# Optimization experiments

Measured on AMD Instinct MI355X. Metric: run time of the kernel, lower is better.

## Reference

```python
import jax, jax.numpy as jnp
import numpy as np

N_NODES = 50000
N_EDGES = 800000
N_GRAPHS = 512
IN_FEATS = 256
HIDDEN = 128
OUT_FEATS = 128


def _lin(key, fan_in, fan_out):
    return jax.random.normal(key, (fan_in, fan_out), jnp.float32) * (1.0 / np.sqrt(fan_in))


def setup_inputs() -> dict:
    key = jax.random.key(0)
    ks = jax.random.split(key, 16)
    x = jax.random.normal(ks[0], (N_NODES, IN_FEATS), jnp.float32)
    edge_index = jax.random.randint(ks[1], (2, N_EDGES), 0, N_NODES, jnp.int32)
    batch = jnp.sort(jax.random.randint(ks[2], (N_NODES,), 0, N_GRAPHS, jnp.int32))
    return {
        "x": x,
        "edge_index": edge_index,
        "batch": batch,
        "num_graphs": N_GRAPHS,
        # TD branch GCN params
        "td_W1": _lin(ks[3], IN_FEATS, HIDDEN), "td_b1": jnp.zeros((HIDDEN,), jnp.float32),
        "td_W2": _lin(ks[4], HIDDEN, OUT_FEATS), "td_b2": jnp.zeros((OUT_FEATS,), jnp.float32),
        # BU branch GCN params
        "bu_W1": _lin(ks[5], IN_FEATS, HIDDEN), "bu_b1": jnp.zeros((HIDDEN,), jnp.float32),
        "bu_W2": _lin(ks[6], HIDDEN, OUT_FEATS), "bu_b2": jnp.zeros((OUT_FEATS,), jnp.float32),
        # proj_head: Linear(256,256) -> ReLU -> Linear(256,128)
        "pw1": _lin(ks[7], OUT_FEATS * 2, 256), "pb1": jnp.zeros((256,), jnp.float32),
        "pw2": _lin(ks[8], 256, 128), "pb2": jnp.zeros((128,), jnp.float32),
    }


def gcn_conv(h_in, W, b, src, dst, n_nodes):
    """PyG GCNConv: self-loops + symmetric normalization D^-1/2 (A+I) D^-1/2 X W + b."""
    h = h_in @ W  # [N, out]
    ones = jnp.ones(src.shape[0], h.dtype)
    deg = jax.ops.segment_sum(ones, dst, num_segments=n_nodes) + 1.0  # +1 for self-loop
    dinv = jax.lax.rsqrt(deg)  # deg >= 1 always
    norm = dinv[src] * dinv[dst]  # [E]
    agg = jax.ops.segment_sum(h[src] * norm[:, None], dst, num_segments=n_nodes)
    agg = agg + h * (dinv * dinv)[:, None]  # self-loop edge contribution
    return agg + b


def reference(x, edge_index, batch, num_graphs,
              td_W1, td_b1, td_W2, td_b2,
              bu_W1, bu_b1, bu_W2, bu_b2,
              pw1, pb1, pw2, pb2):
    n = x.shape[0]
    src, dst = edge_index[0], edge_index[1]

    def branch(W1, b1, W2, b2, s, d):
        h = jax.nn.relu(gcn_conv(x, W1, b1, s, d, n))
        # dropout is identity in eval mode
        h = gcn_conv(h, W2, b2, s, d, n)
        return jax.ops.segment_sum(h, batch, num_segments=num_graphs)  # global_add_pool

    td = branch(td_W1, td_b1, td_W2, td_b2, src, dst)
    bu = branch(bu_W1, bu_b1, bu_W2, bu_b2, dst, src)  # flipped edge_index
    h = jnp.concatenate([bu, td], axis=1)  # [G, 2*out_feats]
    h = jax.nn.relu(h @ pw1 + pb1) @ pw2 + pb2
    return h
```

## Files before the change

### kernel.cpp

```cpp
#include <hip/hip_runtime.h>

#define N_NODES 50000
#define N_PAD   50048
#define N_EDGES 800000
#define N_GRAPHS 512
#define F_IN 256
#define F_H 128
#define F_CAT 256

#define BSHIFT 9
#define NB 98
#define CAP 10240
#define EPB 3125

typedef __attribute__((ext_vector_type(8))) short short8;
typedef __attribute__((ext_vector_type(4))) float f32x4;
typedef unsigned int uint;
typedef unsigned short ushort;

static __device__ __forceinline__ ushort f2bf(float f) {
    uint u = __float_as_uint(f);
    u += 0x7FFF + ((u >> 16) & 1);
    return (ushort)(u >> 16);
}
static __device__ __forceinline__ float bflo(uint v) { return __uint_as_float(v << 16); }
static __device__ __forceinline__ float bfhi(uint v) { return __uint_as_float(v & 0xFFFF0000u); }

#define GLL(g, l) __builtin_amdgcn_global_load_lds( \
    (const __attribute__((address_space(1))) unsigned int*)(g), \
    (__attribute__((address_space(3))) unsigned int*)(l), 16, 0, 0)

__global__ void init_gcur_kernel(int* gcur) {
    int t = threadIdx.x;
    if (t < 2 * NB) gcur[t] = (t % NB) * CAP;
}

__global__ __launch_bounds__(256) void csr_scatter_kernel(
        const int* __restrict__ ei, int* __restrict__ gcur,
        uint* __restrict__ ebuf_td, uint* __restrict__ ebuf_bu) {
    __shared__ int lcnt[256];
    __shared__ int lbase[256];
    int tid = threadIdx.x;
    lcnt[tid] = 0;
    __syncthreads();
    int e0 = blockIdx.x * EPB;
    for (int k = tid; k < EPB; k += 256) {
        int i = e0 + k;
        int s = ei[i], d = ei[N_EDGES + i];
        atomicAdd(&lcnt[d >> BSHIFT], 1);
        atomicAdd(&lcnt[128 + (s >> BSHIFT)], 1);
    }
    __syncthreads();
    if (tid < 2 * NB) {
        int dir = tid / NB, b = tid % NB;
        int c = lcnt[dir * 128 + b];
        lbase[dir * 128 + b] = c ? atomicAdd(&gcur[dir * NB + b], c) : 0;
    }
    __syncthreads();
    lcnt[tid] = 0;
    __syncthreads();
    for (int k = tid; k < EPB; k += 256) {
        int i = e0 + k;
        int s = ei[i], d = ei[N_EDGES + i];
        int bd = d >> BSHIFT, bs = s >> BSHIFT;
        int p = atomicAdd(&lcnt[bd], 1) + lbase[bd];
        ebuf_td[p] = (uint)s | ((uint)(d & 511) << 16);
        int q = atomicAdd(&lcnt[128 + bs], 1) + lbase[128 + bs];
        ebuf_bu[q] = (uint)d | ((uint)(s & 511) << 16);
    }
}

__global__ __launch_bounds__(256) void csr_build_kernel(
        const uint* __restrict__ ebuf_td, const uint* __restrict__ ebuf_bu,
        const int* __restrict__ gcur,
        int* off_td, int* off_bu, ushort* deg_td, ushort* deg_bu,
        float* dinv_td, float* dinv_bu, ushort* csr_td, ushort* csr_bu) {
    int b = blockIdx.x, dir = blockIdx.y;
    const uint* ebuf = dir ? ebuf_bu : ebuf_td;
    int* off     = dir ? off_bu : off_td;
    ushort* deg  = dir ? deg_bu : deg_td;
    float* dinv  = dir ? dinv_bu : dinv_td;
    ushort* csr  = dir ? csr_bu : csr_td;
    __shared__ int cntL[512], offL[512], sm[256];
    int tid = threadIdx.x;
    cntL[tid] = 0; cntL[tid + 256] = 0;
    __syncthreads();
    int rbeg = b * CAP;
    int rend = gcur[dir * NB + b];
    for (int k = rbeg + tid; k < rend; k += 256)
        atomicAdd(&cntL[ebuf[k] >> 16], 1);
    __syncthreads();
    int a0 = cntL[tid * 2], a1 = cntL[tid * 2 + 1];
    int ps = a0 + a1;
    sm[tid] = ps;
    __syncthreads();
    for (int o = 1; o < 256; o <<= 1) {
        int u = (tid >= o) ? sm[tid - o] : 0;
        __syncthreads();
        sm[tid] += u;
        __syncthreads();
    }
    int excl = sm[tid] - ps;
    offL[tid * 2] = excl;
    offL[tid * 2 + 1] = excl + a0;
    __syncthreads();
    int nbase = b << BSHIFT;
#pragma unroll
    for (int j = 0; j < 2; j++) {
        int nloc = tid + j * 256;
        int n = nbase + nloc;
        if (n < N_NODES) {
            off[n] = rbeg + offL[nloc];
            int c = cntL[nloc];
            deg[n] = (ushort)c;
            dinv[n] = rsqrtf((float)c + 1.0f);
        }
    }
    cntL[tid] = offL[tid];
    cntL[tid + 256] = offL[tid + 256];
    __syncthreads();
    for (int k = rbeg + tid; k < rend; k += 256) {
        uint e = ebuf[k];
        int slot = atomicAdd(&cntL[e >> 16], 1);
        csr[rbeg + slot] = (ushort)(e & 0xFFFF);
    }
}

__global__ void cvt_x_kernel(const float* __restrict__ x, ushort* __restrict__ xb) {
    size_t i = (size_t)blockIdx.x * blockDim.x + threadIdx.x;
    ushort4 u = {0, 0, 0, 0};
    if (i < (size_t)N_NODES * (F_IN / 4)) {
        float4 f = ((const float4*)x)[i];
        u.x = f2bf(f.x); u.y = f2bf(f.y); u.z = f2bf(f.z); u.w = f2bf(f.w);
    }
    ((ushort4*)xb)[i] = u;
}

__global__ void prep_w_kernel(const float* __restrict__ td_W1, const float* __restrict__ bu_W1,
                              const float* __restrict__ td_W2, const float* __restrict__ bu_W2,
                              ushort* __restrict__ Bt1, ushort* __restrict__ Bt2) {
    int n = blockIdx.x;
    int k = threadIdx.x;
    float w1 = (n < F_H) ? td_W1[(size_t)k * F_H + n] : bu_W1[(size_t)k * F_H + (n - F_H)];
    Bt1[(size_t)n * 256 + k] = f2bf(w1);
    if (k < 128) {
        float w2 = (n < F_H) ? td_W2[(size_t)k * F_H + n]
                             : bu_W2[(size_t)k * F_H + (n - F_H)];
        Bt2[(size_t)n * 128 + k] = f2bf(w2);
    }
}

__global__ __launch_bounds__(256) void gemm_mfma(
        const ushort* __restrict__ A, const ushort* __restrict__ Bt,
        ushort* __restrict__ C,
        const float* __restrict__ dinv_td, const float* __restrict__ dinv_bu,
        int kLen, int ldb, int aSplit) {
    __shared__ __align__(16) ushort As[128 * 32];
    __shared__ __align__(16) ushort Bs[128 * 32];
    int tid = threadIdx.x;
    int wave = tid >> 6, lane = tid & 63, quad = lane >> 4, l16 = lane & 15;
    size_t bm = (size_t)blockIdx.x * 128;
    size_t bn = (size_t)blockIdx.y * 128;
    const float* dsel = blockIdx.y ? dinv_bu : dinv_td;
    int aOff = aSplit ? (int)bn : 0;

    f32x4 acc[2][8];
    const f32x4 z4 = {0.f, 0.f, 0.f, 0.f};
#pragma unroll
    for (int i = 0; i < 2; i++)
#pragma unroll
        for (int j = 0; j < 8; j++) acc[i][j] = z4;

    int cb0 = wave * 64;
    int cb1 = 256 + wave * 64;
    int c0 = cb0 + lane, c1 = cb1 + lane;
    int r0 = c0 >> 2, s0 = (c0 & 3) * 8;
    int r1 = c1 >> 2, s1 = (c1 & 3) * 8;
    const ushort* a0p = A + (bm + r0) * 256 + aOff + s0;
    const ushort* a1p = A + (bm + r1) * 256 + aOff + s1;
    const ushort* b0p = Bt + (bn + r0) * ldb + s0;
    const ushort* b1p = Bt + (bn + r1) * ldb + s1;
    ushort* lA0 = As + cb0 * 8;
    ushort* lA1 = As + cb1 * 8;
    ushort* lB0 = Bs + cb0 * 8;
    ushort* lB1 = Bs + cb1 * 8;

    int nkb = kLen >> 5;
    for (int kb = 0; kb < nkb; kb++) {
        int k0 = kb * 32;
        __syncthreads();
        GLL(a0p + k0, lA0);
        GLL(a1p + k0, lA1);
        GLL(b0p + k0, lB0);
        GLL(b1p + k0, lB1);
        __syncthreads();
        short8 af0 = *(const short8*)(As + (wave * 32 + l16) * 32 + quad * 8);
        short8 af1 = *(const short8*)(As + (wave * 32 + 16 + l16) * 32 + quad * 8);
#pragma unroll
        for (int ct = 0; ct < 8; ct++) {
            short8 bfr = *(const short8*)(Bs + (ct * 16 + l16) * 32 + quad * 8);
            acc[0][ct] = __builtin_amdgcn_mfma_f32_16x16x32_bf16(af0, bfr, acc[0][ct], 0, 0, 0);
            acc[1][ct] = __builtin_amdgcn_mfma_f32_16x16x32_bf16(af1, bfr, acc[1][ct], 0, 0, 0);
        }
    }
#pragma unroll
    for (int rt = 0; rt < 2; rt++) {
#pragma unroll
        for (int r = 0; r < 4; r++) {
            size_t row = bm + wave * 32 + rt * 16 + quad * 4 + r;
            float dv = dsel[row];
#pragma unroll
            for (int ct = 0; ct < 8; ct++) {
                C[row * 256 + bn + ct * 16 + l16] = f2bf(acc[rt][ct][r] * dv);
            }
        }
    }
}

static __device__ __forceinline__ void gather_row(const ushort* __restrict__ base,
                                                  const ushort* __restrict__ csr,
                                                  int s, int e, float& a0, float& a1) {
    float p0 = 0, p1 = 0, q0 = 0, q1 = 0, r0 = 0, r1 = 0;
    int k = s;
    for (; k + 4 <= e; k += 4) {
        int i0 = csr[k], i1 = csr[k + 1], i2 = csr[k + 2], i3 = csr[k + 3];
        uint v0 = *(const uint*)(base + (size_t)i0 * F_CAT);
        uint v1 = *(const uint*)(base + (size_t)i1 * F_CAT);
        uint v2 = *(const uint*)(base + (size_t)i2 * F_CAT);
        uint v3 = *(const uint*)(base + (size_t)i3 * F_CAT);
        a0 += bflo(v0); a1 += bfhi(v0);
        p0 += bflo(v1); p1 += bfhi(v1);
        q0 += bflo(v2); q1 += bfhi(v2);
        r0 += bflo(v3); r1 += bfhi(v3);
    }
    for (; k < e; k++) {
        int i0 = csr[k];
        uint v0 = *(const uint*)(base + (size_t)i0 * F_CAT);
        a0 += bflo(v0); a1 += bfhi(v0);
    }
    a0 += (p0 + q0) + r0;
    a1 += (p1 + q1) + r1;
}

__global__ __launch_bounds__(128) void agg1_kernel(
        const ushort* __restrict__ linS, ushort* __restrict__ h1b,
        const ushort* __restrict__ csr_td, const int* __restrict__ off_td,
        const ushort* __restrict__ deg_td, const float* __restrict__ dinv_td,
        const ushort* __restrict__ csr_bu, const int* __restrict__ off_bu,
        const ushort* __restrict__ deg_bu, const float* __restrict__ dinv_bu,
        const float* __restrict__ b_td, const float* __restrict__ b_bu) {
    int n = blockIdx.x;
    int br = threadIdx.x >> 6, lane = threadIdx.x & 63;
    const ushort* csr = br ? csr_bu : csr_td;
    const int* off    = br ? off_bu : off_td;
    const ushort* deg = br ? deg_bu : deg_td;
    const float* dinv = br ? dinv_bu : dinv_td;
    const float* bias = br ? b_bu : b_td;
    size_t cbase = (size_t)br * F_H + lane * 2;
    const ushort* base = linS + cbase;

    uint v = *(const uint*)(base + (size_t)n * F_CAT);
    float a0 = bflo(v), a1 = bfhi(v);
    int s = off[n];
    gather_row(base, csr, s, s + deg[n], a0, a1);
    float dn = dinv[n];
    float o0 = fmaxf(a0 * dn + bias[lane * 2], 0.f);
    float o1 = fmaxf(a1 * dn + bias[lane * 2 + 1], 0.f);
    uint pk = (uint)f2bf(o0) | ((uint)f2bf(o1) << 16);
    *(uint*)(h1b + (size_t)n * F_CAT + cbase) = pk;
}

__global__ __launch_bounds__(128) void agg2_pool_kernel(
        const ushort* __restrict__ linS, float* __restrict__ pooled,
        const int* __restrict__ batch,
        const ushort* __restrict__ csr_td, const int* __restrict__ off_td,
        const ushort* __restrict__ deg_td, const float* __restrict__ dinv_td,
        const ushort* __restrict__ csr_bu, const int* __restrict__ off_bu,
        const ushort* __restrict__ deg_bu, const float* __restrict__ dinv_bu,
        const float* __restrict__ b_td, const float* __restrict__ b_bu) {
    int n0 = blockIdx.x * 8;
    int br = threadIdx.x >> 6, lane = threadIdx.x & 63;
    const ushort* csr = br ? csr_bu : csr_td;
    const int* off    = br ? off_bu : off_td;
    const ushort* deg = br ? deg_bu : deg_td;
    const float* dinv = br ? dinv_bu : dinv_td;
    const float* bias = br ? b_bu : b_td;
    size_t cbase = (size_t)br * F_H + lane * 2;
    const ushort* base = linS + cbase;
    int pcol = (br ? 0 : F_H) + lane * 2;
    float bs0 = bias[lane * 2], bs1 = bias[lane * 2 + 1];

    float acc0 = 0.f, acc1 = 0.f;
    int gcur = batch[n0];
#pragma unroll
    for (int j = 0; j < 8; j++) {
        int n = n0 + j;
        int g = batch[n];
        if (g != gcur) {
            unsafeAtomicAdd(&pooled[(size_t)gcur * F_CAT + pcol], acc0);
            unsafeAtomicAdd(&pooled[(size_t)gcur * F_CAT + pcol + 1], acc1);
            acc0 = acc1 = 0.f;
            gcur = g;
        }
        uint v = *(const uint*)(base + (size_t)n * F_CAT);
        float a0 = bflo(v), a1 = bfhi(v);
        int s = off[n];
        gather_row(base, csr, s, s + deg[n], a0, a1);
        float dn = dinv[n];
        acc0 += a0 * dn + bs0;
        acc1 += a1 * dn + bs1;
    }
    unsafeAtomicAdd(&pooled[(size_t)gcur * F_CAT + pcol], acc0);
    unsafeAtomicAdd(&pooled[(size_t)gcur * F_CAT + pcol + 1], acc1);
}

__global__ __launch_bounds__(256) void mlp_kernel(const float* __restrict__ pooled,
                                                  const float* __restrict__ pw1,
                                                  const float* __restrict__ pb1,
                                                  const float* __restrict__ pw2,
                                                  const float* __restrict__ pb2,
                                                  float* __restrict__ out) {
    int g = blockIdx.x;
    int tid = threadIdx.x;
    __shared__ float row[256];
    __shared__ float hid[256];
    row[tid] = pooled[(size_t)g * 256 + tid];
    __syncthreads();
    float acc = pb1[tid];
    for (int k = 0; k < 256; k++) acc += row[k] * pw1[(size_t)k * 256 + tid];
    hid[tid] = fmaxf(acc, 0.f);
    __syncthreads();
    if (tid < 128) {
        float o = pb2[tid];
        for (int k = 0; k < 256; k++) o += hid[k] * pw2[(size_t)k * 128 + tid];
        out[(size_t)g * 128 + tid] = o;
    }
}

extern "C" void kernel_launch(void* const* d_in, const int* in_sizes, int n_in,
                              void* d_out, int out_size, void* d_ws, size_t ws_size,
                              hipStream_t stream) {
    const float* x     = (const float*)d_in[0];
    const int*   ei    = (const int*)d_in[1];
    const int*   batch = (const int*)d_in[2];
    const float* td_W1 = (const float*)d_in[4];
    const float* td_b1 = (const float*)d_in[5];
    const float* td_W2 = (const float*)d_in[6];
    const float* td_b2 = (const float*)d_in[7];
    const float* bu_W1 = (const float*)d_in[8];
    const float* bu_b1 = (const float*)d_in[9];
    const float* bu_W2 = (const float*)d_in[10];
    const float* bu_b2 = (const float*)d_in[11];
    const float* pw1   = (const float*)d_in[12];
    const float* pb1   = (const float*)d_in[13];
    const float* pw2   = (const float*)d_in[14];
    const float* pb2   = (const float*)d_in[15];
    float* out = (float*)d_out;

    char* p = (char*)d_ws;
    auto alloc = [&](size_t bytes) { void* r = (void*)p; p += (bytes + 255) & ~(size_t)255; return r; };
    int* gcur = (int*)alloc(2 * NB * sizeof(int));
    uint* ebuf_td = (uint*)alloc((size_t)NB * CAP * sizeof(uint));
    uint* ebuf_bu = (uint*)alloc((size_t)NB * CAP * sizeof(uint));
    ushort* csr_td = (ushort*)alloc((size_t)NB * CAP * sizeof(ushort));
    ushort* csr_bu = (ushort*)alloc((size_t)NB * CAP * sizeof(ushort));
    int* off_td = (int*)alloc((size_t)N_NODES * sizeof(int));
    int* off_bu = (int*)alloc((size_t)N_NODES * sizeof(int));
    ushort* deg_td = (ushort*)alloc((size_t)N_NODES * sizeof(ushort));
    ushort* deg_bu = (ushort*)alloc((size_t)N_NODES * sizeof(ushort));
    float* dinv_td = (float*)alloc((size_t)N_PAD * sizeof(float));
    float* dinv_bu = (float*)alloc((size_t)N_PAD * sizeof(float));
    ushort* Bt1 = (ushort*)alloc((size_t)256 * 256 * sizeof(ushort));
    ushort* Bt2 = (ushort*)alloc((size_t)256 * 128 * sizeof(ushort));
    ushort* xb   = (ushort*)alloc((size_t)N_PAD * F_CAT * sizeof(ushort));
    ushort* linb = (ushort*)alloc((size_t)N_PAD * F_CAT * sizeof(ushort));
    ushort* h1b  = (ushort*)alloc((size_t)N_PAD * F_CAT * sizeof(ushort));
    float* pooled = (float*)alloc((size_t)N_GRAPHS * F_CAT * sizeof(float));

    hipMemsetAsync(pooled, 0, (size_t)N_GRAPHS * F_CAT * sizeof(float), stream);

    init_gcur_kernel<<<1, 256, 0, stream>>>(gcur);
    csr_scatter_kernel<<<N_EDGES / EPB, 256, 0, stream>>>(ei, gcur, ebuf_td, ebuf_bu);
    csr_build_kernel<<<dim3(NB, 2), 256, 0, stream>>>(ebuf_td, ebuf_bu, gcur,
        off_td, off_bu, deg_td, deg_bu, dinv_td, dinv_bu, csr_td, csr_bu);

    cvt_x_kernel<<<(N_PAD * F_IN / 4) / 256, 256, 0, stream>>>(x, xb);
    prep_w_kernel<<<256, 256, 0, stream>>>(td_W1, bu_W1, td_W2, bu_W2, Bt1, Bt2);

    dim3 gg(N_PAD / 128, 2);

    gemm_mfma<<<gg, 256, 0, stream>>>(xb, Bt1, linb, dinv_td, dinv_bu, 256, 256, 0);
    agg1_kernel<<<N_NODES, 128, 0, stream>>>(linb, h1b,
        csr_td, off_td, deg_td, dinv_td, csr_bu, off_bu, deg_bu, dinv_bu, td_b1, bu_b1);

    gemm_mfma<<<gg, 256, 0, stream>>>(h1b, Bt2, linb, dinv_td, dinv_bu, 128, 128, 1);
    agg2_pool_kernel<<<N_NODES / 8, 128, 0, stream>>>(linb, pooled, batch,
        csr_td, off_td, deg_td, dinv_td, csr_bu, off_bu, deg_bu, dinv_bu, td_b2, bu_b2);

    mlp_kernel<<<N_GRAPHS, 256, 0, stream>>>(pooled, pw1, pb1, pw2, pb2, out);
}
```

Baseline: 372.1 us.

## Split aggregation columns into 32-wide slices with edge-parallel lanes per wave

The aggregation kernels now give each wave one node (or 8-node group) and one 32-column slice. The 64 lanes are split into 4 edge sub-groups of 16 column lanes, and partial sums are combined with cross-lane shuffles. The aim is more memory-level parallelism per node, since 8 edges are loaded concurrently per step instead of one row per lane serially, and better spread of work across blocks. The cost is 64-byte row segments per gather instead of 256-byte ones, idle lanes on low-degree tails, and reloading CSR indices 8 times per node.

```diff
diff --git a/kernel.cpp b/kernel.cpp
--- a/kernel.cpp
+++ b/kernel.cpp
@@ -217,60 +217,51 @@
     }
 }
 
-static __device__ __forceinline__ void gather_row(const ushort* __restrict__ base,
-                                                  const ushort* __restrict__ csr,
-                                                  int s, int e, float& a0, float& a1) {
-    float p0 = 0, p1 = 0, q0 = 0, q1 = 0, r0 = 0, r1 = 0;
-    int k = s;
-    for (; k + 4 <= e; k += 4) {
-        int i0 = csr[k], i1 = csr[k + 1], i2 = csr[k + 2], i3 = csr[k + 3];
-        uint v0 = *(const uint*)(base + (size_t)i0 * F_CAT);
-        uint v1 = *(const uint*)(base + (size_t)i1 * F_CAT);
-        uint v2 = *(const uint*)(base + (size_t)i2 * F_CAT);
-        uint v3 = *(const uint*)(base + (size_t)i3 * F_CAT);
-        a0 += bflo(v0); a1 += bfhi(v0);
-        p0 += bflo(v1); p1 += bfhi(v1);
-        q0 += bflo(v2); q1 += bfhi(v2);
-        r0 += bflo(v3); r1 += bfhi(v3);
-    }
-    for (; k < e; k++) {
-        int i0 = csr[k];
-        uint v0 = *(const uint*)(base + (size_t)i0 * F_CAT);
-        a0 += bflo(v0); a1 += bfhi(v0);
-    }
-    a0 += (p0 + q0) + r0;
-    a1 += (p1 + q1) + r1;
-}
-
-__global__ __launch_bounds__(128) void agg1_kernel(
+__global__ __launch_bounds__(256) void agg1_kernel(
         const ushort* __restrict__ linS, ushort* __restrict__ h1b,
         const ushort* __restrict__ csr_td, const int* __restrict__ off_td,
         const ushort* __restrict__ deg_td, const float* __restrict__ dinv_td,
         const ushort* __restrict__ csr_bu, const int* __restrict__ off_bu,
         const ushort* __restrict__ deg_bu, const float* __restrict__ dinv_bu,
         const float* __restrict__ b_td, const float* __restrict__ b_bu) {
-    int n = blockIdx.x;
-    int br = threadIdx.x >> 6, lane = threadIdx.x & 63;
-    const ushort* csr = br ? csr_bu : csr_td;
-    const int* off    = br ? off_bu : off_td;
-    const ushort* deg = br ? deg_bu : deg_td;
-    const float* dinv = br ? dinv_bu : dinv_td;
-    const float* bias = br ? b_bu : b_td;
-    size_t cbase = (size_t)br * F_H + lane * 2;
-    const ushort* base = linS + cbase;
-
-    uint v = *(const uint*)(base + (size_t)n * F_CAT);
-    float a0 = bflo(v), a1 = bfhi(v);
-    int s = off[n];
-    gather_row(base, csr, s, s + deg[n], a0, a1);
+    int s = blockIdx.x & 7;
+    int wave = threadIdx.x >> 6, lane = threadIdx.x & 63;
+    int n = (blockIdx.x >> 3) * 4 + wave;
+    int dir = s >> 2;
+    const ushort* csr = dir ? csr_bu : csr_td;
+    const int* off    = dir ? off_bu : off_td;
+    const ushort* deg = dir ? deg_bu : deg_td;
+    const float* dinv = dir ? dinv_bu : dinv_td;
+    const float* bias = dir ? b_bu : b_td;
+    int e_sub = lane >> 4, c_sub = lane & 15;
+    int col = s * 32 + c_sub * 2;
+    const ushort* base = linS + col;
+
+    float a0 = 0.f, a1 = 0.f;
+    int kb = off[n], ke = kb + deg[n];
+    for (int k = kb; k < ke; k += 8) {
+        int k1 = k + e_sub, k2 = k + 4 + e_sub;
+        uint v1 = 0, v2 = 0;
+        if (k1 < ke) v1 = *(const uint*)(base + (size_t)csr[k1] * F_CAT);
+        if (k2 < ke) v2 = *(const uint*)(base + (size_t)csr[k2] * F_CAT);
+        a0 += bflo(v1) + bflo(v2);
+        a1 += bfhi(v1) + bfhi(v2);
+    }
+    a0 += __shfl_xor(a0, 16); a1 += __shfl_xor(a1, 16);
+    a0 += __shfl_xor(a0, 32); a1 += __shfl_xor(a1, 32);
+    uint vs = *(const uint*)(base + (size_t)n * F_CAT);
+    a0 += bflo(vs); a1 += bfhi(vs);
     float dn = dinv[n];
-    float o0 = fmaxf(a0 * dn + bias[lane * 2], 0.f);
-    float o1 = fmaxf(a1 * dn + bias[lane * 2 + 1], 0.f);
-    uint pk = (uint)f2bf(o0) | ((uint)f2bf(o1) << 16);
-    *(uint*)(h1b + (size_t)n * F_CAT + cbase) = pk;
-}
-
-__global__ __launch_bounds__(128) void agg2_pool_kernel(
+    int bcol = col - dir * F_H;
+    float o0 = fmaxf(a0 * dn + bias[bcol], 0.f);
+    float o1 = fmaxf(a1 * dn + bias[bcol + 1], 0.f);
+    if (e_sub == 0) {
+        uint pk = (uint)f2bf(o0) | ((uint)f2bf(o1) << 16);
+        *(uint*)(h1b + (size_t)n * F_CAT + col) = pk;
+    }
+}
+
+__global__ __launch_bounds__(256) void agg2_pool_kernel(
         const ushort* __restrict__ linS, float* __restrict__ pooled,
         const int* __restrict__ batch,
         const ushort* __restrict__ csr_td, const int* __restrict__ off_td,
@@ -278,17 +269,22 @@
         const ushort* __restrict__ csr_bu, const int* __restrict__ off_bu,
         const ushort* __restrict__ deg_bu, const float* __restrict__ dinv_bu,
         const float* __restrict__ b_td, const float* __restrict__ b_bu) {
-    int n0 = blockIdx.x * 8;
-    int br = threadIdx.x >> 6, lane = threadIdx.x & 63;
-    const ushort* csr = br ? csr_bu : csr_td;
-    const int* off    = br ? off_bu : off_td;
-    const ushort* deg = br ? deg_bu : deg_td;
-    const float* dinv = br ? dinv_bu : dinv_td;
-    const float* bias = br ? b_bu : b_td;
-    size_t cbase = (size_t)br * F_H + lane * 2;
-    const ushort* base = linS + cbase;
-    int pcol = (br ? 0 : F_H) + lane * 2;
-    float bs0 = bias[lane * 2], bs1 = bias[lane * 2 + 1];
+    int s = blockIdx.x & 7;
+    int wave = threadIdx.x >> 6, lane = threadIdx.x & 63;
+    int n0 = ((blockIdx.x >> 3) * 4 + wave) * 8;
+    if (n0 >= N_NODES) return;
+    int dir = s >> 2;
+    const ushort* csr = dir ? csr_bu : csr_td;
+    const int* off    = dir ? off_bu : off_td;
+    const ushort* deg = dir ? deg_bu : deg_td;
+    const float* dinv = dir ? dinv_bu : dinv_td;
+    const float* bias = dir ? b_bu : b_td;
+    int e_sub = lane >> 4, c_sub = lane & 15;
+    int col = s * 32 + c_sub * 2;
+    int pcol = ((s + 4) & 7) * 32 + c_sub * 2;
+    const ushort* base = linS + col;
+    int bcol = col - dir * F_H;
+    float bs0 = bias[bcol], bs1 = bias[bcol + 1];
 
     float acc0 = 0.f, acc1 = 0.f;
     int gcur = batch[n0];
@@ -297,21 +293,35 @@
         int n = n0 + j;
         int g = batch[n];
         if (g != gcur) {
-            unsafeAtomicAdd(&pooled[(size_t)gcur * F_CAT + pcol], acc0);
-            unsafeAtomicAdd(&pooled[(size_t)gcur * F_CAT + pcol + 1], acc1);
+            if (e_sub == 0) {
+                unsafeAtomicAdd(&pooled[(size_t)gcur * F_CAT + pcol], acc0);
+                unsafeAtomicAdd(&pooled[(size_t)gcur * F_CAT + pcol + 1], acc1);
+            }
             acc0 = acc1 = 0.f;
             gcur = g;
         }
-        uint v = *(const uint*)(base + (size_t)n * F_CAT);
-        float a0 = bflo(v), a1 = bfhi(v);
-        int s = off[n];
-        gather_row(base, csr, s, s + deg[n], a0, a1);
+        float a0 = 0.f, a1 = 0.f;
+        int kb = off[n], ke = kb + deg[n];
+        for (int k = kb; k < ke; k += 8) {
+            int k1 = k + e_sub, k2 = k + 4 + e_sub;
+            uint v1 = 0, v2 = 0;
+            if (k1 < ke) v1 = *(const uint*)(base + (size_t)csr[k1] * F_CAT);
+            if (k2 < ke) v2 = *(const uint*)(base + (size_t)csr[k2] * F_CAT);
+            a0 += bflo(v1) + bflo(v2);
+            a1 += bfhi(v1) + bfhi(v2);
+        }
+        a0 += __shfl_xor(a0, 16); a1 += __shfl_xor(a1, 16);
+        a0 += __shfl_xor(a0, 32); a1 += __shfl_xor(a1, 32);
+        uint vs = *(const uint*)(base + (size_t)n * F_CAT);
+        a0 += bflo(vs); a1 += bfhi(vs);
         float dn = dinv[n];
         acc0 += a0 * dn + bs0;
         acc1 += a1 * dn + bs1;
     }
-    unsafeAtomicAdd(&pooled[(size_t)gcur * F_CAT + pcol], acc0);
-    unsafeAtomicAdd(&pooled[(size_t)gcur * F_CAT + pcol + 1], acc1);
+    if (e_sub == 0) {
+        unsafeAtomicAdd(&pooled[(size_t)gcur * F_CAT + pcol], acc0);
+        unsafeAtomicAdd(&pooled[(size_t)gcur * F_CAT + pcol + 1], acc1);
+    }
 }
 
 __global__ __launch_bounds__(256) void mlp_kernel(const float* __restrict__ pooled,
@@ -390,11 +400,11 @@
     dim3 gg(N_PAD / 128, 2);
 
     gemm_mfma<<<gg, 256, 0, stream>>>(xb, Bt1, linb, dinv_td, dinv_bu, 256, 256, 0);
-    agg1_kernel<<<N_NODES, 128, 0, stream>>>(linb, h1b,
+    agg1_kernel<<<(N_NODES / 4) * 8, 256, 0, stream>>>(linb, h1b,
         csr_td, off_td, deg_td, dinv_td, csr_bu, off_bu, deg_bu, dinv_bu, td_b1, bu_b1);
 
     gemm_mfma<<<gg, 256, 0, stream>>>(h1b, Bt2, linb, dinv_td, dinv_bu, 128, 128, 1);
-    agg2_pool_kernel<<<N_NODES / 8, 128, 0, stream>>>(linb, pooled, batch,
+    agg2_pool_kernel<<<((N_NODES / 8 + 3) / 4) * 8, 256, 0, stream>>>(linb, pooled, batch,
         csr_td, off_td, deg_td, dinv_td, csr_bu, off_bu, deg_bu, dinv_bu, td_b2, bu_b2);
 
     mlp_kernel<<<N_GRAPHS, 256, 0, stream>>>(pooled, pw1, pb1, pw2, pb2, out);
```

Measured after the change: 591.5 us. +59.0%, slower.

## Split edge gathers across wave halves with 8-byte loads; fold init into memset

Applied to the files above, without the earlier changes.

The aggregation kernels now split each wave into two halves. Each half walks alternate edges of a node and loads 4 bf16 features per lane instead of 2. The halves combine their partial sums with a cross-half shuffle, which doubles the in-flight edge loads per node and widens each access. Blocks hold two nodes (or two 8-node groups) each. The gcur init kernel is removed by storing bucket offsets relative to the bucket base and zeroing them together with pooled in one memset, which saves a launch at the cost of one extra index calculation per scatter.

```diff
diff --git a/kernel.cpp b/kernel.cpp
--- a/kernel.cpp
+++ b/kernel.cpp
@@ -30,11 +30,6 @@
     (const __attribute__((address_space(1))) unsigned int*)(g), \
     (__attribute__((address_space(3))) unsigned int*)(l), 16, 0, 0)
 
-__global__ void init_gcur_kernel(int* gcur) {
-    int t = threadIdx.x;
-    if (t < 2 * NB) gcur[t] = (t % NB) * CAP;
-}
-
 __global__ __launch_bounds__(256) void csr_scatter_kernel(
         const int* __restrict__ ei, int* __restrict__ gcur,
         uint* __restrict__ ebuf_td, uint* __restrict__ ebuf_bu) {
@@ -64,9 +59,9 @@
         int s = ei[i], d = ei[N_EDGES + i];
         int bd = d >> BSHIFT, bs = s >> BSHIFT;
         int p = atomicAdd(&lcnt[bd], 1) + lbase[bd];
-        ebuf_td[p] = (uint)s | ((uint)(d & 511) << 16);
+        ebuf_td[(size_t)bd * CAP + p] = (uint)s | ((uint)(d & 511) << 16);
         int q = atomicAdd(&lcnt[128 + bs], 1) + lbase[128 + bs];
-        ebuf_bu[q] = (uint)d | ((uint)(s & 511) << 16);
+        ebuf_bu[(size_t)bs * CAP + q] = (uint)d | ((uint)(s & 511) << 16);
     }
 }
 
@@ -86,7 +81,7 @@
     cntL[tid] = 0; cntL[tid + 256] = 0;
     __syncthreads();
     int rbeg = b * CAP;
-    int rend = gcur[dir * NB + b];
+    int rend = rbeg + gcur[dir * NB + b];
     for (int k = rbeg + tid; k < rend; k += 256)
         atomicAdd(&cntL[ebuf[k] >> 16], 1);
     __syncthreads();
@@ -217,60 +212,79 @@
     }
 }
 
-static __device__ __forceinline__ void gather_row(const ushort* __restrict__ base,
-                                                  const ushort* __restrict__ csr,
-                                                  int s, int e, float& a0, float& a1) {
-    float p0 = 0, p1 = 0, q0 = 0, q1 = 0, r0 = 0, r1 = 0;
-    int k = s;
-    for (; k + 4 <= e; k += 4) {
-        int i0 = csr[k], i1 = csr[k + 1], i2 = csr[k + 2], i3 = csr[k + 3];
-        uint v0 = *(const uint*)(base + (size_t)i0 * F_CAT);
-        uint v1 = *(const uint*)(base + (size_t)i1 * F_CAT);
-        uint v2 = *(const uint*)(base + (size_t)i2 * F_CAT);
-        uint v3 = *(const uint*)(base + (size_t)i3 * F_CAT);
-        a0 += bflo(v0); a1 += bfhi(v0);
-        p0 += bflo(v1); p1 += bfhi(v1);
-        q0 += bflo(v2); q1 += bfhi(v2);
-        r0 += bflo(v3); r1 += bfhi(v3);
-    }
-    for (; k < e; k++) {
-        int i0 = csr[k];
-        uint v0 = *(const uint*)(base + (size_t)i0 * F_CAT);
-        a0 += bflo(v0); a1 += bfhi(v0);
-    }
-    a0 += (p0 + q0) + r0;
-    a1 += (p1 + q1) + r1;
-}
-
-__global__ __launch_bounds__(128) void agg1_kernel(
+static __device__ __forceinline__ void gather_node(
+        const ushort* __restrict__ base, const ushort* __restrict__ csr,
+        int kb, int ke, int half, float a[4]) {
+    float p[4] = {0.f, 0.f, 0.f, 0.f};
+    float q[4] = {0.f, 0.f, 0.f, 0.f};
+    float r[4] = {0.f, 0.f, 0.f, 0.f};
+    int k = kb;
+    for (; k + 8 <= ke; k += 8) {
+        int i0 = csr[k + half];
+        int i1 = csr[k + 2 + half];
+        int i2 = csr[k + 4 + half];
+        int i3 = csr[k + 6 + half];
+        uint2 v0 = *(const uint2*)(base + (size_t)i0 * F_CAT);
+        uint2 v1 = *(const uint2*)(base + (size_t)i1 * F_CAT);
+        uint2 v2 = *(const uint2*)(base + (size_t)i2 * F_CAT);
+        uint2 v3 = *(const uint2*)(base + (size_t)i3 * F_CAT);
+        a[0] += bflo(v0.x); a[1] += bfhi(v0.x); a[2] += bflo(v0.y); a[3] += bfhi(v0.y);
+        p[0] += bflo(v1.x); p[1] += bfhi(v1.x); p[2] += bflo(v1.y); p[3] += bfhi(v1.y);
+        q[0] += bflo(v2.x); q[1] += bfhi(v2.x); q[2] += bflo(v2.y); q[3] += bfhi(v2.y);
+        r[0] += bflo(v3.x); r[1] += bfhi(v3.x); r[2] += bflo(v3.y); r[3] += bfhi(v3.y);
+    }
+    for (; k < ke; k += 2) {
+        int kk = k + half;
+        if (kk < ke) {
+            uint2 v = *(const uint2*)(base + (size_t)csr[kk] * F_CAT);
+            a[0] += bflo(v.x); a[1] += bfhi(v.x); a[2] += bflo(v.y); a[3] += bfhi(v.y);
+        }
+    }
+#pragma unroll
+    for (int j = 0; j < 4; j++) a[j] += (p[j] + q[j]) + r[j];
+}
+
+__global__ __launch_bounds__(256) void agg1_kernel(
         const ushort* __restrict__ linS, ushort* __restrict__ h1b,
         const ushort* __restrict__ csr_td, const int* __restrict__ off_td,
         const ushort* __restrict__ deg_td, const float* __restrict__ dinv_td,
         const ushort* __restrict__ csr_bu, const int* __restrict__ off_bu,
         const ushort* __restrict__ deg_bu, const float* __restrict__ dinv_bu,
         const float* __restrict__ b_td, const float* __restrict__ b_bu) {
-    int n = blockIdx.x;
-    int br = threadIdx.x >> 6, lane = threadIdx.x & 63;
+    int wave = threadIdx.x >> 6, lane = threadIdx.x & 63;
+    int n = blockIdx.x * 2 + (wave >> 1);
+    int br = wave & 1;
     const ushort* csr = br ? csr_bu : csr_td;
     const int* off    = br ? off_bu : off_td;
     const ushort* deg = br ? deg_bu : deg_td;
     const float* dinv = br ? dinv_bu : dinv_td;
     const float* bias = br ? b_bu : b_td;
-    size_t cbase = (size_t)br * F_H + lane * 2;
-    const ushort* base = linS + cbase;
-
-    uint v = *(const uint*)(base + (size_t)n * F_CAT);
-    float a0 = bflo(v), a1 = bfhi(v);
-    int s = off[n];
-    gather_row(base, csr, s, s + deg[n], a0, a1);
+    int half = lane >> 5, l32 = lane & 31;
+    int col = br * F_H + l32 * 4;
+    const ushort* base = linS + col;
+
+    float a[4] = {0.f, 0.f, 0.f, 0.f};
+    int kb = off[n];
+    gather_node(base, csr, kb, kb + deg[n], half, a);
+#pragma unroll
+    for (int j = 0; j < 4; j++) a[j] += __shfl_xor(a[j], 32);
+    uint2 vs = *(const uint2*)(base + (size_t)n * F_CAT);
+    a[0] += bflo(vs.x); a[1] += bfhi(vs.x); a[2] += bflo(vs.y); a[3] += bfhi(vs.y);
     float dn = dinv[n];
-    float o0 = fmaxf(a0 * dn + bias[lane * 2], 0.f);
-    float o1 = fmaxf(a1 * dn + bias[lane * 2 + 1], 0.f);
-    uint pk = (uint)f2bf(o0) | ((uint)f2bf(o1) << 16);
-    *(uint*)(h1b + (size_t)n * F_CAT + cbase) = pk;
-}
-
-__global__ __launch_bounds__(128) void agg2_pool_kernel(
+    int bcol = l32 * 4;
+    float o0 = fmaxf(a[0] * dn + bias[bcol],     0.f);
+    float o1 = fmaxf(a[1] * dn + bias[bcol + 1], 0.f);
+    float o2 = fmaxf(a[2] * dn + bias[bcol + 2], 0.f);
+    float o3 = fmaxf(a[3] * dn + bias[bcol + 3], 0.f);
+    if (half == 0) {
+        uint2 pk;
+        pk.x = (uint)f2bf(o0) | ((uint)f2bf(o1) << 16);
+        pk.y = (uint)f2bf(o2) | ((uint)f2bf(o3) << 16);
+        *(uint2*)(h1b + (size_t)n * F_CAT + col) = pk;
+    }
+}
+
+__global__ __launch_bounds__(256) void agg2_pool_kernel(
         const ushort* __restrict__ linS, float* __restrict__ pooled,
         const int* __restrict__ batch,
         const ushort* __restrict__ csr_td, const int* __restrict__ off_td,
@@ -278,40 +292,59 @@
         const ushort* __restrict__ csr_bu, const int* __restrict__ off_bu,
         const ushort* __restrict__ deg_bu, const float* __restrict__ dinv_bu,
         const float* __restrict__ b_td, const float* __restrict__ b_bu) {
-    int n0 = blockIdx.x * 8;
-    int br = threadIdx.x >> 6, lane = threadIdx.x & 63;
+    int wave = threadIdx.x >> 6, lane = threadIdx.x & 63;
+    int n0 = (blockIdx.x * 2 + (wave >> 1)) * 8;
+    int br = wave & 1;
     const ushort* csr = br ? csr_bu : csr_td;
     const int* off    = br ? off_bu : off_td;
     const ushort* deg = br ? deg_bu : deg_td;
     const float* dinv = br ? dinv_bu : dinv_td;
     const float* bias = br ? b_bu : b_td;
-    size_t cbase = (size_t)br * F_H + lane * 2;
-    const ushort* base = linS + cbase;
-    int pcol = (br ? 0 : F_H) + lane * 2;
-    float bs0 = bias[lane * 2], bs1 = bias[lane * 2 + 1];
-
-    float acc0 = 0.f, acc1 = 0.f;
+    int half = lane >> 5, l32 = lane & 31;
+    int col = br * F_H + l32 * 4;
+    int pcol = (br ? 0 : F_H) + l32 * 4;
+    const ushort* base = linS + col;
+    int bcol = l32 * 4;
+    float bs0 = bias[bcol], bs1 = bias[bcol + 1];
+    float bs2 = bias[bcol + 2], bs3 = bias[bcol + 3];
+
+    float acc0 = 0.f, acc1 = 0.f, acc2 = 0.f, acc3 = 0.f;
     int gcur = batch[n0];
 #pragma unroll
     for (int j = 0; j < 8; j++) {
         int n = n0 + j;
         int g = batch[n];
         if (g != gcur) {
-            unsafeAtomicAdd(&pooled[(size_t)gcur * F_CAT + pcol], acc0);
-            unsafeAtomicAdd(&pooled[(size_t)gcur * F_CAT + pcol + 1], acc1);
-            acc0 = acc1 = 0.f;
+            if (half == 0) {
+                float* pp = &pooled[(size_t)gcur * F_CAT + pcol];
+                unsafeAtomicAdd(pp,     acc0);
+                unsafeAtomicAdd(pp + 1, acc1);
+                unsafeAtomicAdd(pp + 2, acc2);
+                unsafeAtomicAdd(pp + 3, acc3);
+            }
+            acc0 = acc1 = acc2 = acc3 = 0.f;
             gcur = g;
         }
-        uint v = *(const uint*)(base + (size_t)n * F_CAT);
-        float a0 = bflo(v), a1 = bfhi(v);
-        int s = off[n];
-        gather_row(base, csr, s, s + deg[n], a0, a1);
+        float a[4] = {0.f, 0.f, 0.f, 0.f};
+        int kb = off[n];
+        gather_node(base, csr, kb, kb + deg[n], half, a);
+#pragma unroll
+        for (int t = 0; t < 4; t++) a[t] += __shfl_xor(a[t], 32);
+        uint2 vs = *(const uint2*)(base + (size_t)n * F_CAT);
+        a[0] += bflo(vs.x); a[1] += bfhi(vs.x); a[2] += bflo(vs.y); a[3] += bfhi(vs.y);
         float dn = dinv[n];
-        acc0 += a0 * dn + bs0;
-        acc1 += a1 * dn + bs1;
-    }
-    unsafeAtomicAdd(&pooled[(size_t)gcur * F_CAT + pcol], acc0);
-    unsafeAtomicAdd(&pooled[(size_t)gcur * F_CAT + pcol + 1], acc1);
+        acc0 += a[0] * dn + bs0;
+        acc1 += a[1] * dn + bs1;
+        acc2 += a[2] * dn + bs2;
+        acc3 += a[3] * dn + bs3;
+    }
+    if (half == 0) {
+        float* pp = &pooled[(size_t)gcur * F_CAT + pcol];
+        unsafeAtomicAdd(pp,     acc0);
+        unsafeAtomicAdd(pp + 1, acc1);
+        unsafeAtomicAdd(pp + 2, acc2);
+        unsafeAtomicAdd(pp + 3, acc3);
+    }
 }
 
 __global__ __launch_bounds__(256) void mlp_kernel(const float* __restrict__ pooled,
@@ -359,7 +392,9 @@
 
     char* p = (char*)d_ws;
     auto alloc = [&](size_t bytes) { void* r = (void*)p; p += (bytes + 255) & ~(size_t)255; return r; };
-    int* gcur = (int*)alloc(2 * NB * sizeof(int));
+    char* zreg = (char*)alloc(1024 + (size_t)N_GRAPHS * F_CAT * sizeof(float));
+    int* gcur = (int*)zreg;
+    float* pooled = (float*)(zreg + 1024);
     uint* ebuf_td = (uint*)alloc((size_t)NB * CAP * sizeof(uint));
     uint* ebuf_bu = (uint*)alloc((size_t)NB * CAP * sizeof(uint));
     ushort* csr_td = (ushort*)alloc((size_t)NB * CAP * sizeof(ushort));
@@ -375,11 +410,9 @@
     ushort* xb   = (ushort*)alloc((size_t)N_PAD * F_CAT * sizeof(ushort));
     ushort* linb = (ushort*)alloc((size_t)N_PAD * F_CAT * sizeof(ushort));
     ushort* h1b  = (ushort*)alloc((size_t)N_PAD * F_CAT * sizeof(ushort));
-    float* pooled = (float*)alloc((size_t)N_GRAPHS * F_CAT * sizeof(float));
-
-    hipMemsetAsync(pooled, 0, (size_t)N_GRAPHS * F_CAT * sizeof(float), stream);
-
-    init_gcur_kernel<<<1, 256, 0, stream>>>(gcur);
+
+    hipMemsetAsync(zreg, 0, 1024 + (size_t)N_GRAPHS * F_CAT * sizeof(float), stream);
+
     csr_scatter_kernel<<<N_EDGES / EPB, 256, 0, stream>>>(ei, gcur, ebuf_td, ebuf_bu);
     csr_build_kernel<<<dim3(NB, 2), 256, 0, stream>>>(ebuf_td, ebuf_bu, gcur,
         off_td, off_bu, deg_td, deg_bu, dinv_td, dinv_bu, csr_td, csr_bu);
@@ -390,11 +423,11 @@
     dim3 gg(N_PAD / 128, 2);
 
     gemm_mfma<<<gg, 256, 0, stream>>>(xb, Bt1, linb, dinv_td, dinv_bu, 256, 256, 0);
-    agg1_kernel<<<N_NODES, 128, 0, stream>>>(linb, h1b,
+    agg1_kernel<<<N_NODES / 2, 256, 0, stream>>>(linb, h1b,
         csr_td, off_td, deg_td, dinv_td, csr_bu, off_bu, deg_bu, dinv_bu, td_b1, bu_b1);
 
     gemm_mfma<<<gg, 256, 0, stream>>>(h1b, Bt2, linb, dinv_td, dinv_bu, 128, 128, 1);
-    agg2_pool_kernel<<<N_NODES / 8, 128, 0, stream>>>(linb, pooled, batch,
+    agg2_pool_kernel<<<N_NODES / 16, 256, 0, stream>>>(linb, pooled, batch,
         csr_td, off_td, deg_td, dinv_td, csr_bu, off_bu, deg_bu, dinv_bu, td_b2, bu_b2);
 
     mlp_kernel<<<N_GRAPHS, 256, 0, stream>>>(pooled, pw1, pb1, pw2, pb2, out);
```

After: 360.9 us. 1.03x faster.
